# Kernel tuning notes

Hardware: AMD Instinct MI355X
Metric: run time of the kernel (lower is better)

The kernel has to match this reference:

```python
import jax, jax.numpy as jnp
import numpy as np


def setup_inputs() -> dict:
    key = jax.random.key(0)
    ks = jax.random.split(key, 9)
    B, D_in, H, C = 32768, 784, 256, 10
    def lin(k, fan_in, shape):
        return jax.random.normal(k, shape, dtype=jnp.float32) / np.sqrt(fan_in).astype(np.float32)
    return {
        "x": jax.random.normal(ks[0], (B, D_in), dtype=jnp.float32),
        "W1": lin(ks[1], D_in, (H, D_in)),
        "b1": lin(ks[2], D_in, (H,)),
        "W2": lin(ks[3], H, (H, H)),
        "b2": lin(ks[4], H, (H,)),
        "W3": lin(ks[5], H, (H, H)),
        "b3": lin(ks[6], H, (H,)),
        "W4": lin(ks[7], H, (C, H)),
        "b4": lin(ks[8], H, (C,)),
    }


def reference(x, W1, b1, W2, b2, W3, b3, W4, b4):
    # MLPHeb.forward_with_coactivations:
    #   prev_act = (input > 0); at each activation point (after each ReLU and
    #   at the final Linear), curr_act = (x > 0) and coactivation buffer
    #   accumulates sum_s outer(prev_act[s], curr_act[s]) == prev_act.T @ curr_act.
    act = lambda t: (t > 0).astype(t.dtype)

    a0 = act(x)                              # [B, 784]
    h1 = jax.nn.relu(x @ W1.T + b1)          # [B, 256]
    a1 = act(h1)
    c0 = a0.T @ a1                           # [784, 256]

    h2 = jax.nn.relu(h1 @ W2.T + b2)
    a2 = act(h2)
    c1 = a1.T @ a2                           # [256, 256]

    h3 = jax.nn.relu(h2 @ W3.T + b3)
    a3 = act(h3)
    c2 = a2.T @ a3                           # [256, 256]

    logits = h3 @ W4.T + b4                  # [B, 10] (last layer counts as activation point)
    a4 = act(logits)
    c3 = a3.T @ a4                           # [256, 10]

    return logits, c0, c1, c2, c3
```

## Files before the change

kernel.cpp:

```cpp
#include <hip/hip_runtime.h>
#include <hip/hip_bf16.h>

typedef unsigned short u16;
typedef unsigned long long u64;
typedef __bf16 bf16x8 __attribute__((ext_vector_type(8)));
typedef float f32x4 __attribute__((ext_vector_type(4)));

__device__ __forceinline__ void async16(const void* g, void* l) {
  __builtin_amdgcn_global_load_lds((const __attribute__((address_space(1))) void*)g,
                                   (__attribute__((address_space(3))) void*)l, 16, 0, 0);
}
__device__ __forceinline__ u16 f2bf(float f) {
  __hip_bfloat16 h = __float2bfloat16(f);
  u16 u; __builtin_memcpy(&u, &h, 2); return u;
}

__global__ __launch_bounds__(256) void convert_all(
    const float* __restrict__ W1, const float* __restrict__ W2,
    const float* __restrict__ W3, const float* __restrict__ W4,
    u16* __restrict__ w1b, u16* __restrict__ w2b,
    u16* __restrict__ w3b, u16* __restrict__ w4b) {
  int bx = blockIdx.x;
  const float* src; u16* dst; int R, C, Cp, base;
  if (bx < 800)       { src = W1; dst = w1b; R = 256; C = 784; Cp = 800; base = 0; }
  else if (bx < 1056) { src = W2; dst = w2b; R = 256; C = 256; Cp = 256; base = 800; }
  else if (bx < 1312) { src = W3; dst = w3b; R = 256; C = 256; Cp = 256; base = 1056; }
  else                { src = W4; dst = w4b; R = 10;  C = 256; Cp = 256; base = 1312; }
  int idx = (bx - base) * 256 + threadIdx.x;
  int r = idx / Cp, c = idx - r * Cp;
  float v = (r < R && c < C) ? src[(size_t)r * C + c] : 0.0f;
  dst[idx] = f2bf(v);
}

__global__ __launch_bounds__(256) void prep_x(const float* __restrict__ x,
                                              u16* __restrict__ xb,
                                              u64* __restrict__ bits0) {
  __shared__ u16 S[64 * 66];
  const int t = threadIdx.x;
  const int g = blockIdx.x;
  const int chunk = blockIdx.y;
  const int row0 = chunk * 64, col0 = g * 64;

  if (g < 12) {
    #pragma unroll
    for (int i = 0; i < 4; i++) {
      int idx = i * 256 + t;
      int r = idx >> 4, c4 = (idx & 15) * 4;
      float4 v = *(const float4*)(x + (size_t)(row0 + r) * 784 + col0 + c4);
      ushort4 o;
      o.x = f2bf(v.x); o.y = f2bf(v.y); o.z = f2bf(v.z); o.w = f2bf(v.w);
      *(ushort4*)(xb + (size_t)(row0 + r) * 800 + col0 + c4) = o;
      S[r * 66 + c4]     = v.x > 0.0f;
      S[r * 66 + c4 + 1] = v.y > 0.0f;
      S[r * 66 + c4 + 2] = v.z > 0.0f;
      S[r * 66 + c4 + 3] = v.w > 0.0f;
    }
  } else {
    int r = t >> 2, c4 = (t & 3) * 4;
    float4 v = *(const float4*)(x + (size_t)(row0 + r) * 784 + col0 + c4);
    ushort4 o;
    o.x = f2bf(v.x); o.y = f2bf(v.y); o.z = f2bf(v.z); o.w = f2bf(v.w);
    *(ushort4*)(xb + (size_t)(row0 + r) * 800 + col0 + c4) = o;
    ushort4 z = {0, 0, 0, 0};
    *(ushort4*)(xb + (size_t)(row0 + r) * 800 + 784 + c4) = z;
    S[r * 66 + c4]     = v.x > 0.0f;
    S[r * 66 + c4 + 1] = v.y > 0.0f;
    S[r * 66 + c4 + 2] = v.z > 0.0f;
    S[r * 66 + c4 + 3] = v.w > 0.0f;
  }
  __syncthreads();

  const int lane = t & 63, wv = t >> 6;
  const int ncols = (g < 12) ? 64 : 16;
  const int cbase = wv * 16;
  if (cbase < ncols) {
    u64 my = 0;
    #pragma unroll
    for (int i = 0; i < 16; i++) {
      u64 m = __ballot(S[lane * 66 + cbase + i] != 0);
      if (lane == i) my = m;
    }
    if (lane < 16) bits0[(size_t)chunk * 784 + col0 + cbase + lane] = my;
  }
}

__global__ __launch_bounds__(512, 4) void fwd_fused(
    const u16* __restrict__ xb,
    const u16* __restrict__ W1b, const float* __restrict__ b1,
    const u16* __restrict__ W2b, const float* __restrict__ b2,
    const u16* __restrict__ W3b, const float* __restrict__ b3,
    const u16* __restrict__ W4b, const float* __restrict__ b4,
    float* __restrict__ out,
    u64* __restrict__ bits1, u64* __restrict__ bits2,
    u64* __restrict__ bits3, u64* __restrict__ bits4) {

  __shared__ __align__(16) u16 hbuf[8 * 64 * 40];
  __shared__ __align__(16) u16 Wt[2][256 * 32];
  __shared__ __align__(16) u16 At[2][64 * 32];

  const int tid = threadIdx.x;
  const int lane = tid & 63, wv = tid >> 6;
  const int lm = lane & 15, q = lane >> 4;
  const int m0 = blockIdx.x * 64;
  const int wm = (wv & 1) * 32;
  const int wn = (wv >> 1) * 64;

  auto stageW = [&](const u16* W, int K, int kc, u16* dst) {
    #pragma unroll
    for (int i = 0; i < 2; i++) {
      int seg = i * 512 + tid;
      int n = seg >> 2, kq = seg & 3;
      async16(W + (size_t)n * K + kc * 32 + kq * 8, dst + seg * 8);
    }
  };
  auto stageA = [&](int kc, u16* dst) {
    if (tid < 256) {
      int r = tid >> 2, kq = tid & 3;
      async16(xb + (size_t)(m0 + r) * 800 + kc * 32 + kq * 8, dst + tid * 8);
    }
  };
  auto stageW4 = [&]() {
    if (tid < 512) async16(W4b + tid * 8, Wt[1] + tid * 8);
  };
  auto epilogue = [&](f32x4 (&acc)[2][4], const float* __restrict__ bias) {
    #pragma unroll
    for (int mi = 0; mi < 2; mi++) {
      int row = wm + mi * 16 + lm;
      #pragma unroll
      for (int ni = 0; ni < 4; ni++) {
        int col = wn + ni * 16 + q * 4;
        float4 bv = *(const float4*)(bias + col);
        float h0 = acc[mi][ni][0] + bv.x; h0 = h0 > 0.0f ? h0 : 0.0f;
        float h1 = acc[mi][ni][1] + bv.y; h1 = h1 > 0.0f ? h1 : 0.0f;
        float h2 = acc[mi][ni][2] + bv.z; h2 = h2 > 0.0f ? h2 : 0.0f;
        float h3 = acc[mi][ni][3] + bv.w; h3 = h3 > 0.0f ? h3 : 0.0f;
        ushort4 o = {f2bf(h0), f2bf(h1), f2bf(h2), f2bf(h3)};
        int kt = col >> 5, cin = col & 31;
        *(ushort4*)(hbuf + kt * 2560 + row * 40 + cin) = o;
      }
    }
  };
  auto ballot_pass = [&](u64* bits) {
    u64 my = 0;
    #pragma unroll
    for (int g = 0; g < 4; g++) {
      ushort4 v0 = *(const ushort4*)(hbuf + wv * 2560 + lane * 40 + g * 8);
      ushort4 v1 = *(const ushort4*)(hbuf + wv * 2560 + lane * 40 + g * 8 + 4);
      u16 s[8] = {v0.x, v0.y, v0.z, v0.w, v1.x, v1.y, v1.z, v1.w};
      #pragma unroll
      for (int j = 0; j < 8; j++) {
        u64 m = __ballot(s[j] != 0);
        if (lane == g * 8 + j) my = m;
      }
    }
    if (lane < 32) bits[(size_t)blockIdx.x * 256 + wv * 32 + lane] = my;
  };

  {
    f32x4 acc[2][4] = {};
    stageA(0, At[0]);
    stageW(W1b, 800, 0, Wt[0]);
    for (int kc = 0; kc < 25; kc++) {
      int cur = kc & 1;
      __syncthreads();
      if (kc < 24) { stageA(kc + 1, At[1 - cur]); stageW(W1b, 800, kc + 1, Wt[1 - cur]); }
      else         { stageW(W2b, 256, 0, Wt[1]); }
      bf16x8 w[4], h[2];
      #pragma unroll
      for (int ni = 0; ni < 4; ni++) w[ni] = *(const bf16x8*)(Wt[cur] + (wn + ni * 16 + lm) * 32 + q * 8);
      #pragma unroll
      for (int mi = 0; mi < 2; mi++) h[mi] = *(const bf16x8*)(At[cur] + (wm + mi * 16 + lm) * 32 + q * 8);
      #pragma unroll
      for (int mi = 0; mi < 2; mi++)
        #pragma unroll
        for (int ni = 0; ni < 4; ni++)
          acc[mi][ni] = __builtin_amdgcn_mfma_f32_16x16x32_bf16(w[ni], h[mi], acc[mi][ni], 0, 0, 0);
    }
    __syncthreads();
    epilogue(acc, b1);
  }
  __syncthreads();
  ballot_pass(bits1);

  auto layer256 = [&](const u16* Wthis, const u16* Wnext, bool nextIsW4,
                      const float* __restrict__ bias, u64* bits) {
    f32x4 acc[2][4] = {};
    for (int kc = 0; kc < 8; kc++) {
      int cur = (kc & 1) ^ 1;
      __syncthreads();
      if (kc < 7)       stageW(Wthis, 256, kc + 1, Wt[cur ^ 1]);
      else if (nextIsW4) stageW4();
      else              stageW(Wnext, 256, 0, Wt[cur ^ 1]);
      bf16x8 w[4], h[2];
      #pragma unroll
      for (int ni = 0; ni < 4; ni++) w[ni] = *(const bf16x8*)(Wt[cur] + (wn + ni * 16 + lm) * 32 + q * 8);
      #pragma unroll
      for (int mi = 0; mi < 2; mi++) h[mi] = *(const bf16x8*)(hbuf + kc * 2560 + (wm + mi * 16 + lm) * 40 + q * 8);
      #pragma unroll
      for (int mi = 0; mi < 2; mi++)
        #pragma unroll
        for (int ni = 0; ni < 4; ni++)
          acc[mi][ni] = __builtin_amdgcn_mfma_f32_16x16x32_bf16(w[ni], h[mi], acc[mi][ni], 0, 0, 0);
    }
    __syncthreads();
    epilogue(acc, bias);
    __syncthreads();
    ballot_pass(bits);
  };
  layer256(W2b, W3b, false, b2, bits2);
  layer256(W3b, W4b, true,  b3, bits3);

  if (wv < 4) {
    const int r0 = wv * 16;
    f32x4 acc = {};
    #pragma unroll
    for (int kc = 0; kc < 8; kc++) {
      bf16x8 wf = *(const bf16x8*)(Wt[1] + lm * 256 + kc * 32 + q * 8);
      bf16x8 hf = *(const bf16x8*)(hbuf + kc * 2560 + (r0 + lm) * 40 + q * 8);
      acc = __builtin_amdgcn_mfma_f32_16x16x32_bf16(wf, hf, acc, 0, 0, 0);
    }
    int row = r0 + lm;
    float4 v;
    #pragma unroll
    for (int r = 0; r < 4; r++) {
      int c = q * 4 + r;
      float bv = (c < 10) ? b4[c] : 0.0f;
      v[r] = acc[r] + bv;
    }
    float* Ls = (float*)At;
    if (q < 3) *(float4*)(Ls + row * 12 + q * 4) = v;
    size_t ob = (size_t)(m0 + row) * 10;
    if (q < 2) {
      *(float2*)(out + ob + q * 4)     = make_float2(v[0], v[1]);
      *(float2*)(out + ob + q * 4 + 2) = make_float2(v[2], v[3]);
    } else if (q == 2) {
      *(float2*)(out + ob + 8) = make_float2(v[0], v[1]);
    }
  }
  __syncthreads();
  if (wv == 0) {
    const float* Ls = (const float*)At;
    float4 c03 = *(const float4*)(Ls + lane * 12);
    float4 c47 = *(const float4*)(Ls + lane * 12 + 4);
    float2 c89 = *(const float2*)(Ls + lane * 12 + 8);
    float s[10] = {c03.x, c03.y, c03.z, c03.w, c47.x, c47.y, c47.z, c47.w, c89.x, c89.y};
    u64 my = 0;
    #pragma unroll
    for (int c = 0; c < 10; c++) {
      u64 m = __ballot(s[c] > 0.0f);
      if (lane == c) my = m;
    }
    if (lane < 10) bits4[(size_t)blockIdx.x * 10 + lane] = my;
  }
}

__global__ __launch_bounds__(256) void coact_all(
    const u64* __restrict__ bits0, const u64* __restrict__ bits1,
    const u64* __restrict__ bits2, const u64* __restrict__ bits3,
    const u64* __restrict__ bits4, float* __restrict__ out) {
  const int bx = blockIdx.x;
  const u64 *bp, *bc; float* Cm; int FP, FC, i0, j0;
  if (bx < 52)      { bp = bits0; bc = bits1; Cm = out + 327680; FP = 784; FC = 256;
                      i0 = (bx % 13) * 64; j0 = (bx / 13) * 64; }
  else if (bx < 68) { int t = bx - 52; bp = bits1; bc = bits2; Cm = out + 528384; FP = 256; FC = 256;
                      i0 = (t & 3) * 64; j0 = (t >> 2) * 64; }
  else if (bx < 84) { int t = bx - 68; bp = bits2; bc = bits3; Cm = out + 593920; FP = 256; FC = 256;
                      i0 = (t & 3) * 64; j0 = (t >> 2) * 64; }
  else              { int t = bx - 84; bp = bits3; bc = bits4; Cm = out + 659456; FP = 256; FC = 10;
                      i0 = t * 64; j0 = 0; }

  __shared__ u64 Ps[16 * 64];
  __shared__ u64 Cs[16 * 64];
  const int tid = threadIdx.x;
  const int ch0 = blockIdx.y * 32;
  const int ti = tid >> 4, tj = tid & 15;
  unsigned cnt[4][4] = {};

  for (int s = 0; s < 2; s++) {
    int cb = ch0 + s * 16;
    #pragma unroll
    for (int r = 0; r < 4; r++) {
      int l = r * 256 + tid;
      int c = l >> 6, f = l & 63;
      Ps[l] = (i0 + f < FP) ? bp[(size_t)(cb + c) * FP + i0 + f] : 0ULL;
      Cs[l] = (j0 + f < FC) ? bc[(size_t)(cb + c) * FC + j0 + f] : 0ULL;
    }
    __syncthreads();
    #pragma unroll 4
    for (int c = 0; c < 16; c++) {
      u64 pv[4], cv[4];
      #pragma unroll
      for (int a = 0; a < 4; a++) pv[a] = Ps[c * 64 + a * 16 + ti];
      #pragma unroll
      for (int b = 0; b < 4; b++) cv[b] = Cs[c * 64 + b * 16 + tj];
      #pragma unroll
      for (int a = 0; a < 4; a++)
        #pragma unroll
        for (int b = 0; b < 4; b++)
          cnt[a][b] += (unsigned)__builtin_popcountll(pv[a] & cv[b]);
    }
    __syncthreads();
  }

  #pragma unroll
  for (int a = 0; a < 4; a++) {
    int i = i0 + a * 16 + ti;
    if (i >= FP) continue;
    #pragma unroll
    for (int b = 0; b < 4; b++) {
      int j = j0 + b * 16 + tj;
      if (j < FC) atomicAdd(&Cm[(size_t)i * FC + j], (float)cnt[a][b]);
    }
  }
}

extern "C" void kernel_launch(void* const* d_in, const int* in_sizes, int n_in,
                              void* d_out, int out_size, void* d_ws, size_t ws_size,
                              hipStream_t stream) {
  const float* x  = (const float*)d_in[0];
  const float* W1 = (const float*)d_in[1];
  const float* b1 = (const float*)d_in[2];
  const float* W2 = (const float*)d_in[3];
  const float* b2 = (const float*)d_in[4];
  const float* W3 = (const float*)d_in[5];
  const float* b3 = (const float*)d_in[6];
  const float* W4 = (const float*)d_in[7];
  const float* b4 = (const float*)d_in[8];
  float* out = (float*)d_out;

  constexpr size_t O_C0 = 327680, O_END = 662016;

  char* ws = (char*)d_ws;
  u16* xb   = (u16*)(ws);
  char* p = ws + 52428800;
  u16* w1b  = (u16*)p;  p += (size_t)256 * 800 * 2;
  u16* w2b  = (u16*)p;  p += (size_t)256 * 256 * 2;
  u16* w3b  = (u16*)p;  p += (size_t)256 * 256 * 2;
  u16* w4b  = (u16*)p;  p += (size_t)16 * 256 * 2;
  u64* bits0 = (u64*)p; p += (size_t)512 * 784 * 8;
  u64* bits1 = (u64*)p; p += (size_t)512 * 256 * 8;
  u64* bits2 = (u64*)p; p += (size_t)512 * 256 * 8;
  u64* bits3 = (u64*)p; p += (size_t)512 * 256 * 8;
  u64* bits4 = (u64*)p; p += (size_t)512 * 10 * 8;

  hipMemsetAsync((void*)(out + O_C0), 0, (O_END - O_C0) * sizeof(float), stream);

  convert_all<<<1328, 256, 0, stream>>>(W1, W2, W3, W4, w1b, w2b, w3b, w4b);
  prep_x<<<dim3(13, 512), 256, 0, stream>>>(x, xb, bits0);

  fwd_fused<<<512, 512, 0, stream>>>(xb, w1b, b1, w2b, b2, w3b, b3, w4b, b4,
                                     out, bits1, bits2, bits3, bits4);

  coact_all<<<dim3(88, 16), 256, 0, stream>>>(bits0, bits1, bits2, bits3, bits4, out);
}
```

Baseline: 247.6 us.

## Fuse x conversion and input sign-bit packing into the fused forward kernel

Removes the separate prep_x pass, which wrote a bf16 copy of x to workspace. The fused kernel now loads fp32 x straight into registers, converts it to bf16 MFMA fragments, and packs the input activation bits with ballots while the first GEMM runs. This cuts one kernel launch and roughly 50MB of bf16 write plus reread traffic. In exchange the x loads are synchronous per-thread register loads, not async LDS copies. Every K-step also adds ballots and scattered 16-bit stores of bits0.

```diff
diff --git a/kernel.cpp b/kernel.cpp
--- a/kernel.cpp
+++ b/kernel.cpp
@@ -32,71 +32,20 @@
   dst[idx] = f2bf(v);
 }
 
-__global__ __launch_bounds__(256) void prep_x(const float* __restrict__ x,
-                                              u16* __restrict__ xb,
-                                              u64* __restrict__ bits0) {
-  __shared__ u16 S[64 * 66];
-  const int t = threadIdx.x;
-  const int g = blockIdx.x;
-  const int chunk = blockIdx.y;
-  const int row0 = chunk * 64, col0 = g * 64;
-
-  if (g < 12) {
-    #pragma unroll
-    for (int i = 0; i < 4; i++) {
-      int idx = i * 256 + t;
-      int r = idx >> 4, c4 = (idx & 15) * 4;
-      float4 v = *(const float4*)(x + (size_t)(row0 + r) * 784 + col0 + c4);
-      ushort4 o;
-      o.x = f2bf(v.x); o.y = f2bf(v.y); o.z = f2bf(v.z); o.w = f2bf(v.w);
-      *(ushort4*)(xb + (size_t)(row0 + r) * 800 + col0 + c4) = o;
-      S[r * 66 + c4]     = v.x > 0.0f;
-      S[r * 66 + c4 + 1] = v.y > 0.0f;
-      S[r * 66 + c4 + 2] = v.z > 0.0f;
-      S[r * 66 + c4 + 3] = v.w > 0.0f;
-    }
-  } else {
-    int r = t >> 2, c4 = (t & 3) * 4;
-    float4 v = *(const float4*)(x + (size_t)(row0 + r) * 784 + col0 + c4);
-    ushort4 o;
-    o.x = f2bf(v.x); o.y = f2bf(v.y); o.z = f2bf(v.z); o.w = f2bf(v.w);
-    *(ushort4*)(xb + (size_t)(row0 + r) * 800 + col0 + c4) = o;
-    ushort4 z = {0, 0, 0, 0};
-    *(ushort4*)(xb + (size_t)(row0 + r) * 800 + 784 + c4) = z;
-    S[r * 66 + c4]     = v.x > 0.0f;
-    S[r * 66 + c4 + 1] = v.y > 0.0f;
-    S[r * 66 + c4 + 2] = v.z > 0.0f;
-    S[r * 66 + c4 + 3] = v.w > 0.0f;
-  }
-  __syncthreads();
-
-  const int lane = t & 63, wv = t >> 6;
-  const int ncols = (g < 12) ? 64 : 16;
-  const int cbase = wv * 16;
-  if (cbase < ncols) {
-    u64 my = 0;
-    #pragma unroll
-    for (int i = 0; i < 16; i++) {
-      u64 m = __ballot(S[lane * 66 + cbase + i] != 0);
-      if (lane == i) my = m;
-    }
-    if (lane < 16) bits0[(size_t)chunk * 784 + col0 + cbase + lane] = my;
-  }
-}
-
 __global__ __launch_bounds__(512, 4) void fwd_fused(
-    const u16* __restrict__ xb,
+    const float* __restrict__ x,
     const u16* __restrict__ W1b, const float* __restrict__ b1,
     const u16* __restrict__ W2b, const float* __restrict__ b2,
     const u16* __restrict__ W3b, const float* __restrict__ b3,
     const u16* __restrict__ W4b, const float* __restrict__ b4,
     float* __restrict__ out,
-    u64* __restrict__ bits1, u64* __restrict__ bits2,
-    u64* __restrict__ bits3, u64* __restrict__ bits4) {
+    u64* __restrict__ bits0, u64* __restrict__ bits1,
+    u64* __restrict__ bits2, u64* __restrict__ bits3,
+    u64* __restrict__ bits4) {
 
   __shared__ __align__(16) u16 hbuf[8 * 64 * 40];
   __shared__ __align__(16) u16 Wt[2][256 * 32];
-  __shared__ __align__(16) u16 At[2][64 * 32];
+  __shared__ __align__(16) float Ls[64 * 12];
 
   const int tid = threadIdx.x;
   const int lane = tid & 63, wv = tid >> 6;
@@ -111,12 +60,6 @@
       int seg = i * 512 + tid;
       int n = seg >> 2, kq = seg & 3;
       async16(W + (size_t)n * K + kc * 32 + kq * 8, dst + seg * 8);
-    }
-  };
-  auto stageA = [&](int kc, u16* dst) {
-    if (tid < 256) {
-      int r = tid >> 2, kq = tid & 3;
-      async16(xb + (size_t)(m0 + r) * 800 + kc * 32 + kq * 8, dst + tid * 8);
     }
   };
   auto stageW4 = [&]() {
@@ -158,23 +101,71 @@
 
   {
     f32x4 acc[2][4] = {};
-    stageA(0, At[0]);
+    float4 xv[2][2];
+    bf16x8 hA[2];
+    const int arow = m0 + wm + lm;
+
+    auto loadX = [&](int kc) {
+      int col = kc * 32 + q * 8;
+      bool ok = col + 7 < 784;
+      #pragma unroll
+      for (int mi = 0; mi < 2; mi++) {
+        if (ok) {
+          const float* src = x + (size_t)(arow + mi * 16) * 784 + col;
+          xv[mi][0] = *(const float4*)src;
+          xv[mi][1] = *(const float4*)(src + 4);
+        } else {
+          xv[mi][0] = float4{0, 0, 0, 0};
+          xv[mi][1] = float4{0, 0, 0, 0};
+        }
+      }
+    };
+    auto cvtX = [&]() {
+      #pragma unroll
+      for (int mi = 0; mi < 2; mi++) {
+        union { bf16x8 v; u16 s[8]; } u;
+        u.s[0] = f2bf(xv[mi][0].x); u.s[1] = f2bf(xv[mi][0].y);
+        u.s[2] = f2bf(xv[mi][0].z); u.s[3] = f2bf(xv[mi][0].w);
+        u.s[4] = f2bf(xv[mi][1].x); u.s[5] = f2bf(xv[mi][1].y);
+        u.s[6] = f2bf(xv[mi][1].z); u.s[7] = f2bf(xv[mi][1].w);
+        hA[mi] = u.v;
+      }
+    };
+    auto emitBits0 = [&](int kc) {
+      if (wv >= 2) return;
+      u16* b16 = (u16*)bits0;
+      #pragma unroll
+      for (int mi = 0; mi < 2; mi++) {
+        union { bf16x8 v; short s[8]; } u; u.v = hA[mi];
+        int piece = (wm + mi * 16) >> 4;
+        #pragma unroll
+        for (int j = 0; j < 8; j++) {
+          u64 m = __ballot(u.s[j] > 0);
+          int col = kc * 32 + q * 8 + j;
+          if (lm == j && col < 784)
+            b16[((size_t)blockIdx.x * 784 + col) * 4 + piece] = (u16)(m >> (q * 16));
+        }
+      }
+    };
+
     stageW(W1b, 800, 0, Wt[0]);
+    loadX(0);
+    cvtX();
     for (int kc = 0; kc < 25; kc++) {
       int cur = kc & 1;
       __syncthreads();
-      if (kc < 24) { stageA(kc + 1, At[1 - cur]); stageW(W1b, 800, kc + 1, Wt[1 - cur]); }
+      if (kc < 24) { stageW(W1b, 800, kc + 1, Wt[1 - cur]); loadX(kc + 1); }
       else         { stageW(W2b, 256, 0, Wt[1]); }
-      bf16x8 w[4], h[2];
+      bf16x8 w[4];
       #pragma unroll
       for (int ni = 0; ni < 4; ni++) w[ni] = *(const bf16x8*)(Wt[cur] + (wn + ni * 16 + lm) * 32 + q * 8);
-      #pragma unroll
-      for (int mi = 0; mi < 2; mi++) h[mi] = *(const bf16x8*)(At[cur] + (wm + mi * 16 + lm) * 32 + q * 8);
       #pragma unroll
       for (int mi = 0; mi < 2; mi++)
         #pragma unroll
         for (int ni = 0; ni < 4; ni++)
-          acc[mi][ni] = __builtin_amdgcn_mfma_f32_16x16x32_bf16(w[ni], h[mi], acc[mi][ni], 0, 0, 0);
+          acc[mi][ni] = __builtin_amdgcn_mfma_f32_16x16x32_bf16(w[ni], hA[mi], acc[mi][ni], 0, 0, 0);
+      emitBits0(kc);
+      if (kc < 24) cvtX();
     }
     __syncthreads();
     epilogue(acc, b1);
@@ -227,7 +218,6 @@
       float bv = (c < 10) ? b4[c] : 0.0f;
       v[r] = acc[r] + bv;
     }
-    float* Ls = (float*)At;
     if (q < 3) *(float4*)(Ls + row * 12 + q * 4) = v;
     size_t ob = (size_t)(m0 + row) * 10;
     if (q < 2) {
@@ -239,7 +229,6 @@
   }
   __syncthreads();
   if (wv == 0) {
-    const float* Ls = (const float*)At;
     float4 c03 = *(const float4*)(Ls + lane * 12);
     float4 c47 = *(const float4*)(Ls + lane * 12 + 4);
     float2 c89 = *(const float2*)(Ls + lane * 12 + 8);
@@ -330,9 +319,7 @@
 
   constexpr size_t O_C0 = 327680, O_END = 662016;
 
-  char* ws = (char*)d_ws;
-  u16* xb   = (u16*)(ws);
-  char* p = ws + 52428800;
+  char* p = (char*)d_ws;
   u16* w1b  = (u16*)p;  p += (size_t)256 * 800 * 2;
   u16* w2b  = (u16*)p;  p += (size_t)256 * 256 * 2;
   u16* w3b  = (u16*)p;  p += (size_t)256 * 256 * 2;
@@ -346,10 +333,9 @@
   hipMemsetAsync((void*)(out + O_C0), 0, (O_END - O_C0) * sizeof(float), stream);
 
   convert_all<<<1328, 256, 0, stream>>>(W1, W2, W3, W4, w1b, w2b, w3b, w4b);
-  prep_x<<<dim3(13, 512), 256, 0, stream>>>(x, xb, bits0);
-
-  fwd_fused<<<512, 512, 0, stream>>>(xb, w1b, b1, w2b, b2, w3b, b3, w4b, b4,
-                                     out, bits1, bits2, bits3, bits4);
+
+  fwd_fused<<<512, 512, 0, stream>>>(x, w1b, b1, w2b, b2, w3b, b3, w4b, b4,
+                                     out, bits0, bits1, bits2, bits3, bits4);
 
   coact_all<<<dim3(88, 16), 256, 0, stream>>>(bits0, bits1, bits2, bits3, bits4, out);
 }
```

Measured after the change: 258.4 us. 4.4% more time.
